# Performance work log

Hardware: AMD Instinct MI355X
Metric: run time of the kernel (lower is better)

## Reference

```python
import jax, jax.numpy as jnp
import numpy as np
import math

SEQ, BATCH, IN_DIM = 2048, 2, 512
EMBED, HEADS = 512, 8
HEAD_DIM = EMBED // HEADS


def setup_inputs() -> dict:
    key = jax.random.key(0)
    ks = jax.random.split(key, 6)
    # xavier-uniform style init for weights (stored as [in, out])
    def xavier(k, fan_in, fan_out):
        limit = math.sqrt(6.0 / (fan_in + fan_out))
        return jax.random.uniform(k, (fan_in, fan_out), jnp.float32, -limit, limit)
    return {
        "x": jax.random.normal(ks[0], (SEQ, BATCH, IN_DIM), jnp.float32),
        "relative_positional_bias": jax.random.normal(ks[1], (1, HEADS, SEQ, SEQ), jnp.float32),
        "Wqkv": xavier(ks[2], IN_DIM, 3 * EMBED),
        "bqkv": jnp.zeros((3 * EMBED,), jnp.float32),
        "Wo": xavier(ks[3], EMBED, EMBED),
        "bo": jnp.zeros((EMBED,), jnp.float32),
    }


def reference(x, relative_positional_bias, Wqkv, bqkv, Wo, bo):
    # x: [S, B, D] -> [B, S, D]
    xb = jnp.transpose(x, (1, 0, 2))
    B, S, _ = xb.shape
    qkv = xb @ Wqkv + bqkv                       # [B, S, 3E]
    qkv = qkv.reshape(B, S, HEADS, 3 * HEAD_DIM).transpose(0, 2, 1, 3)  # [B,H,S,3hd]
    q, k, v = jnp.split(qkv, 3, axis=-1)         # each [B, H, S, hd]
    # nonstandard scaling: 1/sqrt(2 * d_k)
    scale = 1.0 / math.sqrt(2.0 * HEAD_DIM)
    logits = jnp.einsum("bhqd,bhkd->bhqk", q, k) * scale
    logits = logits + relative_positional_bias   # broadcast over batch
    attn = jax.nn.softmax(logits, axis=-1)
    vals = jnp.einsum("bhqk,bhkd->bhqd", attn, v)  # [B, H, S, hd]
    vals = vals.transpose(0, 2, 1, 3).reshape(B, S, EMBED)
    return vals @ Wo + bo                        # [B, S, E]
```

## Files before the change

### kernel.cpp

```cpp
#include <hip/hip_runtime.h>
#include <hip/hip_bf16.h>

#define SEQ 2048
#define BATCH 2
#define IN_DIM 512
#define EMBED 512
#define HEADS 8
#define HD 64
#define N3 1536

using f32x4 = __attribute__((ext_vector_type(4))) float;
using s16x8 = __attribute__((ext_vector_type(8))) short;

__device__ __forceinline__ unsigned short f2bf(float f) {
    union { float f; unsigned int u; } v; v.f = f;
    unsigned int u = v.u;
    unsigned int r = (u + 0x7FFFu + ((u >> 16) & 1u)) >> 16;
    return (unsigned short)r;
}

__device__ __forceinline__ void async16(void* lds, const void* g) {
    __builtin_amdgcn_global_load_lds(
        (const __attribute__((address_space(1))) unsigned int*)g,
        (__attribute__((address_space(3))) unsigned int*)lds, 16, 0, 0);
}

__global__ __launch_bounds__(256) void prep_x(
    const float* __restrict__ x, unsigned short* __restrict__ Ab)
{
    const int gid = blockIdx.x * 256 + threadIdx.x;
    const int base = gid * 4;
    const int m = base >> 9, k = base & 511;
    const int b = m >> 11, s = m & 2047;
    float4 f = *reinterpret_cast<const float4*>(x + ((size_t)s * BATCH + b) * IN_DIM + k);
    ushort4 u;
    u.x = f2bf(f.x); u.y = f2bf(f.y); u.z = f2bf(f.z); u.w = f2bf(f.w);
    *reinterpret_cast<ushort4*>(Ab + (size_t)m * IN_DIM + k) = u;
}

__global__ __launch_bounds__(256) void transpose_w2(
    const float* __restrict__ Wqkv, const float* __restrict__ Wo,
    unsigned short* __restrict__ Wqkvt, unsigned short* __restrict__ Wot)
{
    __shared__ __align__(16) unsigned short T[64][72];
    const int yy = blockIdx.y;
    const float* in; unsigned short* out; int N, n0;
    if (yy < 24) { in = Wqkv; out = Wqkvt; N = N3;    n0 = yy * 64; }
    else         { in = Wo;   out = Wot;   N = EMBED; n0 = (yy - 24) * 64; }
    const int k0 = blockIdx.x * 64;
    const int tid = threadIdx.x;
    const int ri = tid >> 2, cj = (tid & 3) * 16;
#pragma unroll
    for (int v = 0; v < 4; v++) {
        float4 f = *reinterpret_cast<const float4*>(in + (size_t)(k0 + ri) * N + n0 + cj + 4 * v);
        T[cj + 4 * v + 0][ri] = f2bf(f.x);
        T[cj + 4 * v + 1][ri] = f2bf(f.y);
        T[cj + 4 * v + 2][ri] = f2bf(f.z);
        T[cj + 4 * v + 3][ri] = f2bf(f.w);
    }
    __syncthreads();
    unsigned short* dst = out + (size_t)(n0 + ri) * IN_DIM + k0 + cj;
    *reinterpret_cast<uint4*>(dst)     = *reinterpret_cast<const uint4*>(&T[ri][cj]);
    *reinterpret_cast<uint4*>(dst + 8) = *reinterpret_cast<const uint4*>(&T[ri][cj + 8]);
}

__global__ __launch_bounds__(256) void qkv_gemm(
    const unsigned short* __restrict__ Ab, const unsigned short* __restrict__ Wt,
    const float* __restrict__ bqkv,
    unsigned short* __restrict__ Qb, unsigned short* __restrict__ Kb,
    unsigned short* __restrict__ Vt)
{
    __shared__ __align__(16) unsigned short As[64 * 64];
    __shared__ __align__(16) unsigned short Bs[128 * 64];
    const int tid = threadIdx.x, lane = tid & 63, w = tid >> 6;
    const int fr = lane & 15, fg = lane >> 4;
    const int m0 = blockIdx.x * 64, n0 = blockIdx.y * 128;
    const int sr = lane >> 3;
    const int scs = ((lane & 7) * 16) ^ (sr << 4);

    const unsigned char* Ag = (const unsigned char*)Ab + (size_t)(m0 + w * 8 + sr) * 1024 + scs;
    const unsigned char* Bg = (const unsigned char*)Wt + (size_t)(n0 + w * 8 + sr) * 1024 + scs;
    unsigned char* Asb = (unsigned char*)As;
    unsigned char* Bsb = (unsigned char*)Bs;

    f32x4 acc[2][4];
#pragma unroll
    for (int mt = 0; mt < 2; mt++)
#pragma unroll
        for (int nt = 0; nt < 4; nt++) acc[mt][nt] = (f32x4){0.f, 0.f, 0.f, 0.f};

    const int swz = (fr & 7) << 4;

    for (int k0 = 0; k0 < IN_DIM; k0 += 64) {
        async16(Asb + (w * 8) * 128,        Ag);
        async16(Asb + (32 + w * 8) * 128,   Ag + (size_t)32 * 1024);
        async16(Bsb + (w * 8) * 128,        Bg);
        async16(Bsb + (32 + w * 8) * 128,   Bg + (size_t)32 * 1024);
        async16(Bsb + (64 + w * 8) * 128,   Bg + (size_t)64 * 1024);
        async16(Bsb + (96 + w * 8) * 128,   Bg + (size_t)96 * 1024);
        Ag += 128; Bg += 128;
        __syncthreads();
#pragma unroll
        for (int h2 = 0; h2 < 2; h2++) {
            const int cb = (h2 * 64 + fg * 16) ^ swz;
            s16x8 a[2], bf[4];
#pragma unroll
            for (int mt = 0; mt < 2; mt++) {
                const int row = (w >> 1) * 32 + mt * 16 + fr;
                a[mt] = *reinterpret_cast<const s16x8*>(Asb + row * 128 + cb);
            }
#pragma unroll
            for (int nt = 0; nt < 4; nt++) {
                const int nrow = (w & 1) * 64 + nt * 16 + fr;
                bf[nt] = *reinterpret_cast<const s16x8*>(Bsb + nrow * 128 + cb);
            }
#pragma unroll
            for (int mt = 0; mt < 2; mt++)
#pragma unroll
                for (int nt = 0; nt < 4; nt++)
                    acc[mt][nt] = __builtin_amdgcn_mfma_f32_16x16x32_bf16(a[mt], bf[nt], acc[mt][nt], 0, 0, 0);
        }
        __syncthreads();
    }

    const int wc = w & 1, wr = w >> 1;
    const int b_ = m0 >> 11;
    const int sB = (m0 & 2047) + wr * 32;
#pragma unroll
    for (int nt = 0; nt < 4; nt++) {
        const int col0 = n0 + wc * 64 + nt * 16;
        const int g = col0 >> 6;
        const int hh = g / 3, part = g % 3;
        const int d = (col0 & 63) + fr;
        const float bq = bqkv[col0 + fr];
        if (part < 2) {
            unsigned short* dst = (part == 0 ? Qb : Kb) + ((size_t)b_ * HEADS + hh) * SEQ * HD;
#pragma unroll
            for (int mt = 0; mt < 2; mt++)
#pragma unroll
                for (int j = 0; j < 4; j++) {
                    const int s = sB + mt * 16 + fg * 4 + j;
                    dst[(size_t)s * HD + d] = f2bf(acc[mt][nt][j] + bq);
                }
        } else {
            unsigned short* dst = Vt + (((size_t)b_ * HEADS + hh) * HD + d) * SEQ;
#pragma unroll
            for (int mt = 0; mt < 2; mt++) {
                ushort4 u;
                u.x = f2bf(acc[mt][nt][0] + bq);
                u.y = f2bf(acc[mt][nt][1] + bq);
                u.z = f2bf(acc[mt][nt][2] + bq);
                u.w = f2bf(acc[mt][nt][3] + bq);
                *reinterpret_cast<ushort4*>(&dst[sB + mt * 16 + fg * 4]) = u;
            }
        }
    }
}

template<int NSPL>
__global__ __launch_bounds__(256) void flash_attn(
    const unsigned short* __restrict__ Qb, const unsigned short* __restrict__ Kb,
    const unsigned short* __restrict__ Vt, const float* __restrict__ bias,
    unsigned short* __restrict__ Ob, float* __restrict__ Opart,
    float* __restrict__ Mpart, float* __restrict__ Lpart)
{
    __shared__ __align__(16) unsigned short Ks[2][64][72];
    __shared__ __align__(16) unsigned short Vs[2][64][72];
    __shared__ __align__(16) unsigned short Ps[4][16][72];
    const int h = blockIdx.y;
    const int z = blockIdx.z;
    const int b  = (NSPL == 2) ? (z >> 1) : z;
    const int sp = (NSPL == 2) ? (z & 1) : 0;
    const int NST = (NSPL == 2) ? 16 : 32;
    const int kst = sp * (SEQ / NSPL);
    const int q0 = blockIdx.x * 64;
    const int tid = threadIdx.x, lane = tid & 63, w = tid >> 6;
    const int fr = lane & 15, fg = lane >> 4;

    const unsigned short* Kbase = Kb + (size_t)(b * HEADS + h) * SEQ * HD;
    const unsigned short* Vbase = Vt + (size_t)(b * HEADS + h) * HD * SEQ;
    const float* bbase = bias + (size_t)h * SEQ * SEQ + (size_t)q0 * SEQ;

    const unsigned short* qrow = Qb + ((size_t)(b * HEADS + h) * SEQ + q0 + w * 16 + fr) * HD;
    s16x8 qf0 = *reinterpret_cast<const s16x8*>(qrow + fg * 8);
    s16x8 qf1 = *reinterpret_cast<const s16x8*>(qrow + 32 + fg * 8);

    const int r0 = tid >> 3, c0 = (tid & 7) * 8;
    const int r1 = r0 + 32;

    uint4 kr0, kr1, vr0, vr1;
    f32x4 bA[4], bB[4];
    const float* brow = bbase + (size_t)(w * 16 + fr) * SEQ;

    kr0 = *reinterpret_cast<const uint4*>(Kbase + (size_t)(kst + r0) * HD + c0);
    kr1 = *reinterpret_cast<const uint4*>(Kbase + (size_t)(kst + r1) * HD + c0);
    vr0 = *reinterpret_cast<const uint4*>(Vbase + (size_t)r0 * SEQ + kst + c0);
    vr1 = *reinterpret_cast<const uint4*>(Vbase + (size_t)r1 * SEQ + kst + c0);
#pragma unroll
    for (int t = 0; t < 4; t++)
        bA[t] = *reinterpret_cast<const f32x4*>(brow + kst + t * 16 + fg * 4);
    *reinterpret_cast<uint4*>(&Ks[0][r0][c0]) = kr0;
    *reinterpret_cast<uint4*>(&Ks[0][r1][c0]) = kr1;
    *reinterpret_cast<uint4*>(&Vs[0][r0][c0]) = vr0;
    *reinterpret_cast<uint4*>(&Vs[0][r1][c0]) = vr1;
    __syncthreads();

    float mrow = -1e30f, lrow = 0.f;
    f32x4 oacc[4];
#pragma unroll
    for (int t = 0; t < 4; t++) oacc[t] = (f32x4){0.f, 0.f, 0.f, 0.f};

    const float scale = 0.08838834764831845f;

    auto body = [&](int n, const f32x4 (&bc)[4], f32x4 (&bnx)[4]) {
        const int cur = n & 1;
        const bool pf = (n < NST - 1);
        const int kn = kst + (n + 1) * 64;
        if (pf) {
            kr0 = *reinterpret_cast<const uint4*>(Kbase + (size_t)(kn + r0) * HD + c0);
            kr1 = *reinterpret_cast<const uint4*>(Kbase + (size_t)(kn + r1) * HD + c0);
            vr0 = *reinterpret_cast<const uint4*>(Vbase + (size_t)r0 * SEQ + kn + c0);
            vr1 = *reinterpret_cast<const uint4*>(Vbase + (size_t)r1 * SEQ + kn + c0);
#pragma unroll
            for (int t = 0; t < 4; t++)
                bnx[t] = *reinterpret_cast<const f32x4*>(brow + kn + t * 16 + fg * 4);
        }
        f32x4 p[4];
#pragma unroll
        for (int t = 0; t < 4; t++) p[t] = (f32x4){0.f, 0.f, 0.f, 0.f};
#pragma unroll
        for (int h2 = 0; h2 < 2; h2++) {
            s16x8 qf = (h2 == 0) ? qf0 : qf1;
#pragma unroll
            for (int t = 0; t < 4; t++) {
                s16x8 kf = *reinterpret_cast<const s16x8*>(&Ks[cur][t * 16 + fr][h2 * 32 + fg * 8]);
                p[t] = __builtin_amdgcn_mfma_f32_16x16x32_bf16(kf, qf, p[t], 0, 0, 0);
            }
        }
#pragma unroll
        for (int t = 0; t < 4; t++)
#pragma unroll
            for (int j = 0; j < 4; j++)
                p[t][j] = p[t][j] * scale + bc[t][j];
        float tm = fmaxf(fmaxf(fmaxf(p[0][0], p[0][1]), fmaxf(p[0][2], p[0][3])),
                         fmaxf(fmaxf(p[1][0], p[1][1]), fmaxf(p[1][2], p[1][3])));
        tm = fmaxf(tm, fmaxf(fmaxf(fmaxf(p[2][0], p[2][1]), fmaxf(p[2][2], p[2][3])),
                             fmaxf(fmaxf(p[3][0], p[3][1]), fmaxf(p[3][2], p[3][3]))));
        tm = fmaxf(tm, __shfl_xor(tm, 16, 64));
        tm = fmaxf(tm, __shfl_xor(tm, 32, 64));
        const float newm = fmaxf(mrow, tm);
        const float fac = __expf(mrow - newm);
        mrow = newm;
#pragma unroll
        for (int t = 0; t < 4; t++)
#pragma unroll
            for (int j = 0; j < 4; j++)
                p[t][j] = __expf(p[t][j] - mrow);
        float ts = (p[0][0] + p[0][1] + p[0][2] + p[0][3]) + (p[1][0] + p[1][1] + p[1][2] + p[1][3])
                 + (p[2][0] + p[2][1] + p[2][2] + p[2][3]) + (p[3][0] + p[3][1] + p[3][2] + p[3][3]);
        ts += __shfl_xor(ts, 16, 64);
        ts += __shfl_xor(ts, 32, 64);
        lrow = lrow * fac + ts;
#pragma unroll
        for (int t = 0; t < 4; t++) {
            ushort4 u;
            u.x = f2bf(p[t][0]); u.y = f2bf(p[t][1]); u.z = f2bf(p[t][2]); u.w = f2bf(p[t][3]);
            *reinterpret_cast<ushort4*>(&Ps[w][fr][t * 16 + fg * 4]) = u;
        }
#pragma unroll
        for (int t = 0; t < 4; t++)
#pragma unroll
            for (int j = 0; j < 4; j++)
                oacc[t][j] *= fac;
#pragma unroll
        for (int h2 = 0; h2 < 2; h2++) {
            s16x8 pa = *reinterpret_cast<const s16x8*>(&Ps[w][fr][h2 * 32 + fg * 8]);
#pragma unroll
            for (int t = 0; t < 4; t++) {
                s16x8 vf = *reinterpret_cast<const s16x8*>(&Vs[cur][t * 16 + fr][h2 * 32 + fg * 8]);
                oacc[t] = __builtin_amdgcn_mfma_f32_16x16x32_bf16(vf, pa, oacc[t], 0, 0, 0);
            }
        }
        if (pf) {
            const int nxt = cur ^ 1;
            *reinterpret_cast<uint4*>(&Ks[nxt][r0][c0]) = kr0;
            *reinterpret_cast<uint4*>(&Ks[nxt][r1][c0]) = kr1;
            *reinterpret_cast<uint4*>(&Vs[nxt][r0][c0]) = vr0;
            *reinterpret_cast<uint4*>(&Vs[nxt][r1][c0]) = vr1;
        }
        __syncthreads();
    };

    for (int n = 0; n < NST; n += 2) {
        body(n, bA, bB);
        body(n + 1, bB, bA);
    }

    if (NSPL == 1) {
        const float inv = 1.f / lrow;
        unsigned short* dst = Ob + ((size_t)b * SEQ + q0 + w * 16 + fr) * EMBED + h * HD;
#pragma unroll
        for (int t = 0; t < 4; t++) {
            ushort4 u;
            u.x = f2bf(oacc[t][0] * inv); u.y = f2bf(oacc[t][1] * inv);
            u.z = f2bf(oacc[t][2] * inv); u.w = f2bf(oacc[t][3] * inv);
            *reinterpret_cast<ushort4*>(dst + t * 16 + fg * 4) = u;
        }
    } else {
        const int tile = (z * HEADS + h) * 32 + blockIdx.x;
        float* Op = Opart + (size_t)tile * 4096 + (w * 16 + fr) * 64;
#pragma unroll
        for (int t = 0; t < 4; t++)
            *reinterpret_cast<f32x4*>(Op + t * 16 + fg * 4) = oacc[t];
        if (fg == 0) {
            Mpart[tile * 64 + w * 16 + fr] = mrow;
            Lpart[tile * 64 + w * 16 + fr] = lrow;
        }
    }
}

__global__ __launch_bounds__(256) void combine(
    const float* __restrict__ Opart, const float* __restrict__ Mpart,
    const float* __restrict__ Lpart, unsigned short* __restrict__ Ob)
{
    const int qt = blockIdx.x, h = blockIdx.y, b = blockIdx.z;
    const int t = threadIdx.x;
    const int q = t >> 2, dc = (t & 3) * 16;
    const int t0 = ((b * 2 + 0) * HEADS + h) * 32 + qt;
    const int t1 = ((b * 2 + 1) * HEADS + h) * 32 + qt;
    const float m1 = Mpart[t0 * 64 + q], l1 = Lpart[t0 * 64 + q];
    const float m2 = Mpart[t1 * 64 + q], l2 = Lpart[t1 * 64 + q];
    const float M = fmaxf(m1, m2);
    const float w1 = __expf(m1 - M), w2 = __expf(m2 - M);
    const float inv = 1.f / (w1 * l1 + w2 * l2);
    const float* o1 = Opart + (size_t)t0 * 4096 + q * 64 + dc;
    const float* o2 = Opart + (size_t)t1 * 4096 + q * 64 + dc;
    unsigned short* dst = Ob + ((size_t)b * SEQ + qt * 64 + q) * EMBED + h * HD + dc;
#pragma unroll
    for (int v = 0; v < 4; v++) {
        f32x4 a = *reinterpret_cast<const f32x4*>(o1 + 4 * v);
        f32x4 c = *reinterpret_cast<const f32x4*>(o2 + 4 * v);
        ushort4 u;
        u.x = f2bf((w1 * a[0] + w2 * c[0]) * inv);
        u.y = f2bf((w1 * a[1] + w2 * c[1]) * inv);
        u.z = f2bf((w1 * a[2] + w2 * c[2]) * inv);
        u.w = f2bf((w1 * a[3] + w2 * c[3]) * inv);
        *reinterpret_cast<ushort4*>(dst + 4 * v) = u;
    }
}

__global__ __launch_bounds__(256) void out_gemm(
    const unsigned short* __restrict__ Ao, const unsigned short* __restrict__ Wot,
    const float* __restrict__ bo, float* __restrict__ out)
{
    __shared__ __align__(16) unsigned short As[64 * 64];
    __shared__ __align__(16) unsigned short Bs[128 * 64];
    const int tid = threadIdx.x, lane = tid & 63, w = tid >> 6;
    const int fr = lane & 15, fg = lane >> 4;
    const int m0 = blockIdx.x * 64, n0 = blockIdx.y * 128;
    const int sr = lane >> 3;
    const int scs = ((lane & 7) * 16) ^ (sr << 4);

    const unsigned char* Ag = (const unsigned char*)Ao  + (size_t)(m0 + w * 8 + sr) * 1024 + scs;
    const unsigned char* Bg = (const unsigned char*)Wot + (size_t)(n0 + w * 8 + sr) * 1024 + scs;
    unsigned char* Asb = (unsigned char*)As;
    unsigned char* Bsb = (unsigned char*)Bs;

    f32x4 acc[2][4];
#pragma unroll
    for (int mt = 0; mt < 2; mt++)
#pragma unroll
        for (int nt = 0; nt < 4; nt++) acc[mt][nt] = (f32x4){0.f, 0.f, 0.f, 0.f};

    const int swz = (fr & 7) << 4;

    for (int k0 = 0; k0 < EMBED; k0 += 64) {
        async16(Asb + (w * 8) * 128,        Ag);
        async16(Asb + (32 + w * 8) * 128,   Ag + (size_t)32 * 1024);
        async16(Bsb + (w * 8) * 128,        Bg);
        async16(Bsb + (32 + w * 8) * 128,   Bg + (size_t)32 * 1024);
        async16(Bsb + (64 + w * 8) * 128,   Bg + (size_t)64 * 1024);
        async16(Bsb + (96 + w * 8) * 128,   Bg + (size_t)96 * 1024);
        Ag += 128; Bg += 128;
        __syncthreads();
#pragma unroll
        for (int h2 = 0; h2 < 2; h2++) {
            const int cb = (h2 * 64 + fg * 16) ^ swz;
            s16x8 a[2], bf[4];
#pragma unroll
            for (int mt = 0; mt < 2; mt++) {
                const int row = (w >> 1) * 32 + mt * 16 + fr;
                a[mt] = *reinterpret_cast<const s16x8*>(Asb + row * 128 + cb);
            }
#pragma unroll
            for (int nt = 0; nt < 4; nt++) {
                const int nrow = (w & 1) * 64 + nt * 16 + fr;
                bf[nt] = *reinterpret_cast<const s16x8*>(Bsb + nrow * 128 + cb);
            }
#pragma unroll
            for (int mt = 0; mt < 2; mt++)
#pragma unroll
                for (int nt = 0; nt < 4; nt++)
                    acc[mt][nt] = __builtin_amdgcn_mfma_f32_16x16x32_bf16(a[mt], bf[nt], acc[mt][nt], 0, 0, 0);
        }
        __syncthreads();
    }

    const int wc = w & 1, wr = w >> 1;
#pragma unroll
    for (int nt = 0; nt < 4; nt++) {
        const int col = n0 + wc * 64 + nt * 16 + fr;
        const float bb = bo[col];
#pragma unroll
        for (int mt = 0; mt < 2; mt++)
#pragma unroll
            for (int j = 0; j < 4; j++) {
                const int m = m0 + wr * 32 + mt * 16 + fg * 4 + j;
                out[(size_t)m * EMBED + col] = acc[mt][nt][j] + bb;
            }
    }
}

extern "C" void kernel_launch(void* const* d_in, const int* in_sizes, int n_in,
                              void* d_out, int out_size, void* d_ws, size_t ws_size,
                              hipStream_t stream) {
    const float* x    = (const float*)d_in[0];
    const float* bias = (const float*)d_in[1];
    const float* Wqkv = (const float*)d_in[2];
    const float* bqkv = (const float*)d_in[3];
    const float* Wo   = (const float*)d_in[4];
    const float* bo   = (const float*)d_in[5];
    float* out = (float*)d_out;

    const size_t perT = (size_t)BATCH * HEADS * SEQ * HD;
    unsigned short* Qb    = (unsigned short*)d_ws;
    unsigned short* Kb    = Qb + perT;
    unsigned short* Vt    = Kb + perT;
    unsigned short* Ob    = Vt + perT;
    unsigned short* Ab    = Ob + perT;
    unsigned short* Wqkvt = Ab + (size_t)BATCH * SEQ * IN_DIM;
    unsigned short* Wot   = Wqkvt + (size_t)N3 * IN_DIM;
    const size_t base_bytes = (size_t)(5 * perT + (size_t)N3 * IN_DIM + (size_t)EMBED * EMBED) * 2;
    float* Opart = (float*)((unsigned char*)d_ws + base_bytes);
    float* Mpart = Opart + (size_t)4 * HEADS * 32 * 4096;
    float* Lpart = Mpart + (size_t)4 * HEADS * 32 * 64;
    const size_t need = base_bytes + ((size_t)4 * HEADS * 32 * 4096 + (size_t)2 * 4 * HEADS * 32 * 64) * 4;
    const bool split = (ws_size >= need);

    prep_x<<<2048, 256, 0, stream>>>(x, Ab);
    transpose_w2<<<dim3(8, 32), 256, 0, stream>>>(Wqkv, Wo, Wqkvt, Wot);
    qkv_gemm<<<dim3(64, 12), 256, 0, stream>>>(Ab, Wqkvt, bqkv, Qb, Kb, Vt);
    if (split) {
        flash_attn<2><<<dim3(32, 8, 4), 256, 0, stream>>>(Qb, Kb, Vt, bias, Ob, Opart, Mpart, Lpart);
        combine<<<dim3(32, 8, 2), 256, 0, stream>>>(Opart, Mpart, Lpart, Ob);
    } else {
        flash_attn<1><<<dim3(32, 8, 2), 256, 0, stream>>>(Qb, Kb, Vt, bias, Ob, Opart, Mpart, Lpart);
    }
    out_gemm<<<dim3(64, 4), 256, 0, stream>>>(Ob, Wot, bo, out);
}
```

Measured before the change: 269.9 us.

## Share bias tile across both batches in flash attention with 4-way KV split

Each attention block now handles both batch elements for one head and a 128-row query tile, using 512 threads. This lets the large relative-position bias tile be loaded once and used for both batches. The KV range is split four ways, with a new combine4 kernel merging the partials, and the P conversion uses packed bf16 convert instructions. In exchange, K/V shared-memory double buffering is dropped in favour of two barriers per step. The larger partial-output workspace may fail the size check and fall back to the unsplit path with few blocks.

After: 389.4 us. 1.44x slower.

```diff
diff --git a/kernel.cpp b/kernel.cpp
--- a/kernel.cpp
+++ b/kernel.cpp
@@ -158,7 +158,7 @@
 }
 
 template<int NSPL>
-__global__ __launch_bounds__(256) void flash_attn(
+__global__ __launch_bounds__(512, 4) void flash_attn(
     const unsigned short* __restrict__ Qb, const unsigned short* __restrict__ Kb,
     const unsigned short* __restrict__ Vt, const float* __restrict__ bias,
     unsigned short* __restrict__ Ob, float* __restrict__ Opart,
@@ -166,185 +166,213 @@
 {
     __shared__ __align__(16) unsigned short Ks[2][64][72];
     __shared__ __align__(16) unsigned short Vs[2][64][72];
-    __shared__ __align__(16) unsigned short Ps[4][16][72];
+    __shared__ __align__(16) unsigned short Ps[8][16][72];
     const int h = blockIdx.y;
-    const int z = blockIdx.z;
-    const int b  = (NSPL == 2) ? (z >> 1) : z;
-    const int sp = (NSPL == 2) ? (z & 1) : 0;
-    const int NST = (NSPL == 2) ? 16 : 32;
+    const int sp = (NSPL == 4) ? blockIdx.z : 0;
+    const int NST = (NSPL == 4) ? 8 : 32;
     const int kst = sp * (SEQ / NSPL);
-    const int q0 = blockIdx.x * 64;
+    const int qx = blockIdx.x;
+    const int q0 = qx * 128;
     const int tid = threadIdx.x, lane = tid & 63, w = tid >> 6;
     const int fr = lane & 15, fg = lane >> 4;
-
-    const unsigned short* Kbase = Kb + (size_t)(b * HEADS + h) * SEQ * HD;
-    const unsigned short* Vbase = Vt + (size_t)(b * HEADS + h) * HD * SEQ;
-    const float* bbase = bias + (size_t)h * SEQ * SEQ + (size_t)q0 * SEQ;
-
-    const unsigned short* qrow = Qb + ((size_t)(b * HEADS + h) * SEQ + q0 + w * 16 + fr) * HD;
-    s16x8 qf0 = *reinterpret_cast<const s16x8*>(qrow + fg * 8);
-    s16x8 qf1 = *reinterpret_cast<const s16x8*>(qrow + 32 + fg * 8);
-
-    const int r0 = tid >> 3, c0 = (tid & 7) * 8;
-    const int r1 = r0 + 32;
-
-    uint4 kr0, kr1, vr0, vr1;
+    const int sr = tid >> 3, sc8 = (tid & 7) * 8;
+
+    const unsigned short* K0 = Kb + (size_t)(0 * HEADS + h) * SEQ * HD;
+    const unsigned short* K1 = Kb + (size_t)(1 * HEADS + h) * SEQ * HD;
+    const unsigned short* V0 = Vt + (size_t)(0 * HEADS + h) * HD * SEQ;
+    const unsigned short* V1 = Vt + (size_t)(1 * HEADS + h) * HD * SEQ;
+    const float* brow = bias + (size_t)h * SEQ * SEQ + (size_t)(q0 + w * 16 + fr) * SEQ;
+
+    s16x8 qf[2][2];
+#pragma unroll
+    for (int b = 0; b < 2; b++) {
+        const unsigned short* qrow = Qb + ((size_t)(b * HEADS + h) * SEQ + q0 + w * 16 + fr) * HD;
+        qf[b][0] = *reinterpret_cast<const s16x8*>(qrow + fg * 8);
+        qf[b][1] = *reinterpret_cast<const s16x8*>(qrow + 32 + fg * 8);
+    }
+
     f32x4 bA[4], bB[4];
-    const float* brow = bbase + (size_t)(w * 16 + fr) * SEQ;
-
-    kr0 = *reinterpret_cast<const uint4*>(Kbase + (size_t)(kst + r0) * HD + c0);
-    kr1 = *reinterpret_cast<const uint4*>(Kbase + (size_t)(kst + r1) * HD + c0);
-    vr0 = *reinterpret_cast<const uint4*>(Vbase + (size_t)r0 * SEQ + kst + c0);
-    vr1 = *reinterpret_cast<const uint4*>(Vbase + (size_t)r1 * SEQ + kst + c0);
-#pragma unroll
-    for (int t = 0; t < 4; t++)
-        bA[t] = *reinterpret_cast<const f32x4*>(brow + kst + t * 16 + fg * 4);
-    *reinterpret_cast<uint4*>(&Ks[0][r0][c0]) = kr0;
-    *reinterpret_cast<uint4*>(&Ks[0][r1][c0]) = kr1;
-    *reinterpret_cast<uint4*>(&Vs[0][r0][c0]) = vr0;
-    *reinterpret_cast<uint4*>(&Vs[0][r1][c0]) = vr1;
+    {
+        uint4 k0r = *reinterpret_cast<const uint4*>(K0 + (size_t)(kst + sr) * HD + sc8);
+        uint4 k1r = *reinterpret_cast<const uint4*>(K1 + (size_t)(kst + sr) * HD + sc8);
+        uint4 v0r = *reinterpret_cast<const uint4*>(V0 + (size_t)sr * SEQ + kst + sc8);
+        uint4 v1r = *reinterpret_cast<const uint4*>(V1 + (size_t)sr * SEQ + kst + sc8);
+#pragma unroll
+        for (int t = 0; t < 4; t++)
+            bA[t] = *reinterpret_cast<const f32x4*>(brow + kst + t * 16 + fg * 4);
+        *reinterpret_cast<uint4*>(&Ks[0][sr][sc8]) = k0r;
+        *reinterpret_cast<uint4*>(&Ks[1][sr][sc8]) = k1r;
+        *reinterpret_cast<uint4*>(&Vs[0][sr][sc8]) = v0r;
+        *reinterpret_cast<uint4*>(&Vs[1][sr][sc8]) = v1r;
+    }
     __syncthreads();
 
-    float mrow = -1e30f, lrow = 0.f;
-    f32x4 oacc[4];
-#pragma unroll
-    for (int t = 0; t < 4; t++) oacc[t] = (f32x4){0.f, 0.f, 0.f, 0.f};
+    float mrow[2] = {-1e30f, -1e30f}, lrow[2] = {0.f, 0.f};
+    f32x4 oacc[2][4];
+#pragma unroll
+    for (int b = 0; b < 2; b++)
+#pragma unroll
+        for (int t = 0; t < 4; t++) oacc[b][t] = (f32x4){0.f, 0.f, 0.f, 0.f};
 
     const float scale = 0.08838834764831845f;
 
     auto body = [&](int n, const f32x4 (&bc)[4], f32x4 (&bnx)[4]) {
-        const int cur = n & 1;
         const bool pf = (n < NST - 1);
-        const int kn = kst + (n + 1) * 64;
+        const int kt = kst + (n + 1) * 64;
+        uint4 k0r, k1r, v0r, v1r;
         if (pf) {
-            kr0 = *reinterpret_cast<const uint4*>(Kbase + (size_t)(kn + r0) * HD + c0);
-            kr1 = *reinterpret_cast<const uint4*>(Kbase + (size_t)(kn + r1) * HD + c0);
-            vr0 = *reinterpret_cast<const uint4*>(Vbase + (size_t)r0 * SEQ + kn + c0);
-            vr1 = *reinterpret_cast<const uint4*>(Vbase + (size_t)r1 * SEQ + kn + c0);
+            k0r = *reinterpret_cast<const uint4*>(K0 + (size_t)(kt + sr) * HD + sc8);
+            k1r = *reinterpret_cast<const uint4*>(K1 + (size_t)(kt + sr) * HD + sc8);
+            v0r = *reinterpret_cast<const uint4*>(V0 + (size_t)sr * SEQ + kt + sc8);
+            v1r = *reinterpret_cast<const uint4*>(V1 + (size_t)sr * SEQ + kt + sc8);
 #pragma unroll
             for (int t = 0; t < 4; t++)
-                bnx[t] = *reinterpret_cast<const f32x4*>(brow + kn + t * 16 + fg * 4);
-        }
-        f32x4 p[4];
-#pragma unroll
-        for (int t = 0; t < 4; t++) p[t] = (f32x4){0.f, 0.f, 0.f, 0.f};
-#pragma unroll
-        for (int h2 = 0; h2 < 2; h2++) {
-            s16x8 qf = (h2 == 0) ? qf0 : qf1;
+                bnx[t] = *reinterpret_cast<const f32x4*>(brow + kt + t * 16 + fg * 4);
+        }
+#pragma unroll
+        for (int b = 0; b < 2; b++) {
+            f32x4 p[4];
+#pragma unroll
+            for (int t = 0; t < 4; t++) p[t] = (f32x4){0.f, 0.f, 0.f, 0.f};
+#pragma unroll
+            for (int h2 = 0; h2 < 2; h2++) {
+                s16x8 q8 = qf[b][h2];
+#pragma unroll
+                for (int t = 0; t < 4; t++) {
+                    s16x8 kf = *reinterpret_cast<const s16x8*>(&Ks[b][t * 16 + fr][h2 * 32 + fg * 8]);
+                    p[t] = __builtin_amdgcn_mfma_f32_16x16x32_bf16(kf, q8, p[t], 0, 0, 0);
+                }
+            }
+#pragma unroll
+            for (int t = 0; t < 4; t++)
+#pragma unroll
+                for (int j = 0; j < 4; j++)
+                    p[t][j] = p[t][j] * scale + bc[t][j];
+            float tm = fmaxf(fmaxf(fmaxf(p[0][0], p[0][1]), fmaxf(p[0][2], p[0][3])),
+                             fmaxf(fmaxf(p[1][0], p[1][1]), fmaxf(p[1][2], p[1][3])));
+            tm = fmaxf(tm, fmaxf(fmaxf(fmaxf(p[2][0], p[2][1]), fmaxf(p[2][2], p[2][3])),
+                                 fmaxf(fmaxf(p[3][0], p[3][1]), fmaxf(p[3][2], p[3][3]))));
+            tm = fmaxf(tm, __shfl_xor(tm, 16, 64));
+            tm = fmaxf(tm, __shfl_xor(tm, 32, 64));
+            const float newm = fmaxf(mrow[b], tm);
+            const float fac = __expf(mrow[b] - newm);
+            mrow[b] = newm;
+#pragma unroll
+            for (int t = 0; t < 4; t++)
+#pragma unroll
+                for (int j = 0; j < 4; j++)
+                    p[t][j] = __expf(p[t][j] - newm);
+            float ts = (p[0][0] + p[0][1] + p[0][2] + p[0][3]) + (p[1][0] + p[1][1] + p[1][2] + p[1][3])
+                     + (p[2][0] + p[2][1] + p[2][2] + p[2][3]) + (p[3][0] + p[3][1] + p[3][2] + p[3][3]);
+            ts += __shfl_xor(ts, 16, 64);
+            ts += __shfl_xor(ts, 32, 64);
+            lrow[b] = lrow[b] * fac + ts;
 #pragma unroll
             for (int t = 0; t < 4; t++) {
-                s16x8 kf = *reinterpret_cast<const s16x8*>(&Ks[cur][t * 16 + fr][h2 * 32 + fg * 8]);
-                p[t] = __builtin_amdgcn_mfma_f32_16x16x32_bf16(kf, qf, p[t], 0, 0, 0);
-            }
-        }
-#pragma unroll
-        for (int t = 0; t < 4; t++)
-#pragma unroll
-            for (int j = 0; j < 4; j++)
-                p[t][j] = p[t][j] * scale + bc[t][j];
-        float tm = fmaxf(fmaxf(fmaxf(p[0][0], p[0][1]), fmaxf(p[0][2], p[0][3])),
-                         fmaxf(fmaxf(p[1][0], p[1][1]), fmaxf(p[1][2], p[1][3])));
-        tm = fmaxf(tm, fmaxf(fmaxf(fmaxf(p[2][0], p[2][1]), fmaxf(p[2][2], p[2][3])),
-                             fmaxf(fmaxf(p[3][0], p[3][1]), fmaxf(p[3][2], p[3][3]))));
-        tm = fmaxf(tm, __shfl_xor(tm, 16, 64));
-        tm = fmaxf(tm, __shfl_xor(tm, 32, 64));
-        const float newm = fmaxf(mrow, tm);
-        const float fac = __expf(mrow - newm);
-        mrow = newm;
-#pragma unroll
-        for (int t = 0; t < 4; t++)
-#pragma unroll
-            for (int j = 0; j < 4; j++)
-                p[t][j] = __expf(p[t][j] - mrow);
-        float ts = (p[0][0] + p[0][1] + p[0][2] + p[0][3]) + (p[1][0] + p[1][1] + p[1][2] + p[1][3])
-                 + (p[2][0] + p[2][1] + p[2][2] + p[2][3]) + (p[3][0] + p[3][1] + p[3][2] + p[3][3]);
-        ts += __shfl_xor(ts, 16, 64);
-        ts += __shfl_xor(ts, 32, 64);
-        lrow = lrow * fac + ts;
-#pragma unroll
-        for (int t = 0; t < 4; t++) {
-            ushort4 u;
-            u.x = f2bf(p[t][0]); u.y = f2bf(p[t][1]); u.z = f2bf(p[t][2]); u.w = f2bf(p[t][3]);
-            *reinterpret_cast<ushort4*>(&Ps[w][fr][t * 16 + fg * 4]) = u;
-        }
-#pragma unroll
-        for (int t = 0; t < 4; t++)
-#pragma unroll
-            for (int j = 0; j < 4; j++)
-                oacc[t][j] *= fac;
-#pragma unroll
-        for (int h2 = 0; h2 < 2; h2++) {
-            s16x8 pa = *reinterpret_cast<const s16x8*>(&Ps[w][fr][h2 * 32 + fg * 8]);
+                unsigned int lo, hi;
+                asm("v_cvt_pk_bf16_f32 %0, %1, %2" : "=v"(lo) : "v"(p[t][0]), "v"(p[t][1]));
+                asm("v_cvt_pk_bf16_f32 %0, %1, %2" : "=v"(hi) : "v"(p[t][2]), "v"(p[t][3]));
+                uint2 u; u.x = lo; u.y = hi;
+                *reinterpret_cast<uint2*>(&Ps[w][fr][t * 16 + fg * 4]) = u;
+            }
+#pragma unroll
+            for (int t = 0; t < 4; t++)
+#pragma unroll
+                for (int j = 0; j < 4; j++)
+                    oacc[b][t][j] *= fac;
+#pragma unroll
+            for (int h2 = 0; h2 < 2; h2++) {
+                s16x8 pa = *reinterpret_cast<const s16x8*>(&Ps[w][fr][h2 * 32 + fg * 8]);
+#pragma unroll
+                for (int t = 0; t < 4; t++) {
+                    s16x8 vf = *reinterpret_cast<const s16x8*>(&Vs[b][t * 16 + fr][h2 * 32 + fg * 8]);
+                    oacc[b][t] = __builtin_amdgcn_mfma_f32_16x16x32_bf16(vf, pa, oacc[b][t], 0, 0, 0);
+                }
+            }
+        }
+        __syncthreads();
+        if (pf) {
+            *reinterpret_cast<uint4*>(&Ks[0][sr][sc8]) = k0r;
+            *reinterpret_cast<uint4*>(&Ks[1][sr][sc8]) = k1r;
+            *reinterpret_cast<uint4*>(&Vs[0][sr][sc8]) = v0r;
+            *reinterpret_cast<uint4*>(&Vs[1][sr][sc8]) = v1r;
+        }
+        __syncthreads();
+    };
+
+    for (int it = 0; it < NST; it += 2) {
+        body(it, bA, bB);
+        body(it + 1, bB, bA);
+    }
+
+    if (NSPL == 1) {
+#pragma unroll
+        for (int b = 0; b < 2; b++) {
+            const float inv = 1.f / lrow[b];
+            unsigned short* dst = Ob + ((size_t)b * SEQ + q0 + w * 16 + fr) * EMBED + h * HD;
 #pragma unroll
             for (int t = 0; t < 4; t++) {
-                s16x8 vf = *reinterpret_cast<const s16x8*>(&Vs[cur][t * 16 + fr][h2 * 32 + fg * 8]);
-                oacc[t] = __builtin_amdgcn_mfma_f32_16x16x32_bf16(vf, pa, oacc[t], 0, 0, 0);
-            }
-        }
-        if (pf) {
-            const int nxt = cur ^ 1;
-            *reinterpret_cast<uint4*>(&Ks[nxt][r0][c0]) = kr0;
-            *reinterpret_cast<uint4*>(&Ks[nxt][r1][c0]) = kr1;
-            *reinterpret_cast<uint4*>(&Vs[nxt][r0][c0]) = vr0;
-            *reinterpret_cast<uint4*>(&Vs[nxt][r1][c0]) = vr1;
-        }
-        __syncthreads();
-    };
-
-    for (int n = 0; n < NST; n += 2) {
-        body(n, bA, bB);
-        body(n + 1, bB, bA);
-    }
-
-    if (NSPL == 1) {
-        const float inv = 1.f / lrow;
-        unsigned short* dst = Ob + ((size_t)b * SEQ + q0 + w * 16 + fr) * EMBED + h * HD;
-#pragma unroll
-        for (int t = 0; t < 4; t++) {
-            ushort4 u;
-            u.x = f2bf(oacc[t][0] * inv); u.y = f2bf(oacc[t][1] * inv);
-            u.z = f2bf(oacc[t][2] * inv); u.w = f2bf(oacc[t][3] * inv);
-            *reinterpret_cast<ushort4*>(dst + t * 16 + fg * 4) = u;
+                ushort4 u;
+                u.x = f2bf(oacc[b][t][0] * inv); u.y = f2bf(oacc[b][t][1] * inv);
+                u.z = f2bf(oacc[b][t][2] * inv); u.w = f2bf(oacc[b][t][3] * inv);
+                *reinterpret_cast<ushort4*>(dst + t * 16 + fg * 4) = u;
+            }
         }
     } else {
-        const int tile = (z * HEADS + h) * 32 + blockIdx.x;
-        float* Op = Opart + (size_t)tile * 4096 + (w * 16 + fr) * 64;
-#pragma unroll
-        for (int t = 0; t < 4; t++)
-            *reinterpret_cast<f32x4*>(Op + t * 16 + fg * 4) = oacc[t];
-        if (fg == 0) {
-            Mpart[tile * 64 + w * 16 + fr] = mrow;
-            Lpart[tile * 64 + w * 16 + fr] = lrow;
-        }
-    }
-}
-
-__global__ __launch_bounds__(256) void combine(
+        const int tile = (sp * HEADS + h) * 16 + qx;
+#pragma unroll
+        for (int b = 0; b < 2; b++) {
+            float* Op = Opart + ((size_t)(tile * 2 + b) * 128 + w * 16 + fr) * 64;
+#pragma unroll
+            for (int t = 0; t < 4; t++)
+                *reinterpret_cast<f32x4*>(Op + t * 16 + fg * 4) = oacc[b][t];
+            if (fg == 0) {
+                Mpart[(tile * 2 + b) * 128 + w * 16 + fr] = mrow[b];
+                Lpart[(tile * 2 + b) * 128 + w * 16 + fr] = lrow[b];
+            }
+        }
+    }
+}
+
+__global__ __launch_bounds__(256) void combine4(
     const float* __restrict__ Opart, const float* __restrict__ Mpart,
     const float* __restrict__ Lpart, unsigned short* __restrict__ Ob)
 {
     const int qt = blockIdx.x, h = blockIdx.y, b = blockIdx.z;
-    const int t = threadIdx.x;
-    const int q = t >> 2, dc = (t & 3) * 16;
-    const int t0 = ((b * 2 + 0) * HEADS + h) * 32 + qt;
-    const int t1 = ((b * 2 + 1) * HEADS + h) * 32 + qt;
-    const float m1 = Mpart[t0 * 64 + q], l1 = Lpart[t0 * 64 + q];
-    const float m2 = Mpart[t1 * 64 + q], l2 = Lpart[t1 * 64 + q];
-    const float M = fmaxf(m1, m2);
-    const float w1 = __expf(m1 - M), w2 = __expf(m2 - M);
-    const float inv = 1.f / (w1 * l1 + w2 * l2);
-    const float* o1 = Opart + (size_t)t0 * 4096 + q * 64 + dc;
-    const float* o2 = Opart + (size_t)t1 * 4096 + q * 64 + dc;
-    unsigned short* dst = Ob + ((size_t)b * SEQ + qt * 64 + q) * EMBED + h * HD + dc;
-#pragma unroll
-    for (int v = 0; v < 4; v++) {
-        f32x4 a = *reinterpret_cast<const f32x4*>(o1 + 4 * v);
-        f32x4 c = *reinterpret_cast<const f32x4*>(o2 + 4 * v);
+    const int tid = threadIdx.x;
+    const int q = tid >> 1, dc = (tid & 1) * 32;
+    float m[4], l[4];
+#pragma unroll
+    for (int s = 0; s < 4; s++) {
+        const int tile = (s * HEADS + h) * 16 + qt;
+        m[s] = Mpart[(tile * 2 + b) * 128 + q];
+        l[s] = Lpart[(tile * 2 + b) * 128 + q];
+    }
+    const float M = fmaxf(fmaxf(m[0], m[1]), fmaxf(m[2], m[3]));
+    float ws[4], L = 0.f;
+#pragma unroll
+    for (int s = 0; s < 4; s++) { ws[s] = __expf(m[s] - M); L += ws[s] * l[s]; }
+    const float inv = 1.f / L;
+    f32x4 acc[8];
+#pragma unroll
+    for (int v = 0; v < 8; v++) acc[v] = (f32x4){0.f, 0.f, 0.f, 0.f};
+#pragma unroll
+    for (int s = 0; s < 4; s++) {
+        const int tile = (s * HEADS + h) * 16 + qt;
+        const float* src = Opart + ((size_t)(tile * 2 + b) * 128 + q) * 64 + dc;
+#pragma unroll
+        for (int v = 0; v < 8; v++) {
+            f32x4 o = *reinterpret_cast<const f32x4*>(src + 4 * v);
+#pragma unroll
+            for (int j = 0; j < 4; j++) acc[v][j] += ws[s] * o[j];
+        }
+    }
+    unsigned short* dst = Ob + ((size_t)b * SEQ + qt * 128 + q) * EMBED + h * HD + dc;
+#pragma unroll
+    for (int v = 0; v < 8; v++) {
         ushort4 u;
-        u.x = f2bf((w1 * a[0] + w2 * c[0]) * inv);
-        u.y = f2bf((w1 * a[1] + w2 * c[1]) * inv);
-        u.z = f2bf((w1 * a[2] + w2 * c[2]) * inv);
-        u.w = f2bf((w1 * a[3] + w2 * c[3]) * inv);
+        u.x = f2bf(acc[v][0] * inv); u.y = f2bf(acc[v][1] * inv);
+        u.z = f2bf(acc[v][2] * inv); u.w = f2bf(acc[v][3] * inv);
         *reinterpret_cast<ushort4*>(dst + 4 * v) = u;
     }
 }
@@ -442,19 +470,20 @@
     unsigned short* Wot   = Wqkvt + (size_t)N3 * IN_DIM;
     const size_t base_bytes = (size_t)(5 * perT + (size_t)N3 * IN_DIM + (size_t)EMBED * EMBED) * 2;
     float* Opart = (float*)((unsigned char*)d_ws + base_bytes);
-    float* Mpart = Opart + (size_t)4 * HEADS * 32 * 4096;
-    float* Lpart = Mpart + (size_t)4 * HEADS * 32 * 64;
-    const size_t need = base_bytes + ((size_t)4 * HEADS * 32 * 4096 + (size_t)2 * 4 * HEADS * 32 * 64) * 4;
+    const size_t opart_elems = (size_t)4 * HEADS * 16 * 2 * 128 * 64;
+    float* Mpart = Opart + opart_elems;
+    float* Lpart = Mpart + (size_t)4 * HEADS * 16 * 2 * 128;
+    const size_t need = base_bytes + (opart_elems + (size_t)2 * 4 * HEADS * 16 * 2 * 128) * 4;
     const bool split = (ws_size >= need);
 
     prep_x<<<2048, 256, 0, stream>>>(x, Ab);
     transpose_w2<<<dim3(8, 32), 256, 0, stream>>>(Wqkv, Wo, Wqkvt, Wot);
     qkv_gemm<<<dim3(64, 12), 256, 0, stream>>>(Ab, Wqkvt, bqkv, Qb, Kb, Vt);
     if (split) {
-        flash_attn<2><<<dim3(32, 8, 4), 256, 0, stream>>>(Qb, Kb, Vt, bias, Ob, Opart, Mpart, Lpart);
-        combine<<<dim3(32, 8, 2), 256, 0, stream>>>(Opart, Mpart, Lpart, Ob);
+        flash_attn<4><<<dim3(16, 8, 4), 512, 0, stream>>>(Qb, Kb, Vt, bias, Ob, Opart, Mpart, Lpart);
+        combine4<<<dim3(16, 8, 2), 256, 0, stream>>>(Opart, Mpart, Lpart, Ob);
     } else {
-        flash_attn<1><<<dim3(32, 8, 2), 256, 0, stream>>>(Qb, Kb, Vt, bias, Ob, Opart, Mpart, Lpart);
+        flash_attn<1><<<dim3(16, 8, 1), 512, 0, stream>>>(Qb, Kb, Vt, bias, Ob, Opart, Mpart, Lpart);
     }
     out_gemm<<<dim3(64, 4), 256, 0, stream>>>(Ob, Wot, bo, out);
 }
```
